# Optimization experiments

Measured on AMD Instinct MI355X. Metric: run time of the kernel, lower is better.

The kernel has to match this reference:

```python
import jax, jax.numpy as jnp
import numpy as np

N, E = 100000, 3200000
IN, HID, OUT = 512, 256, 64
K, ALPHA = 10, 0.1


def setup_inputs() -> dict:
    key = jax.random.key(0)
    k1, k2, k3, k4, k5, k6 = jax.random.split(key, 6)
    x = jax.random.normal(k1, (N, IN), dtype=jnp.float32)
    edge_index = jax.random.randint(k2, (2, E), 0, N, dtype=jnp.int64)
    s1 = 1.0 / np.sqrt(IN)
    s2 = 1.0 / np.sqrt(HID)
    # nn.Linear default init: U(-1/sqrt(fan_in), 1/sqrt(fan_in))
    W1 = jax.random.uniform(k3, (IN, HID), jnp.float32, -s1, s1)
    b1 = jax.random.uniform(k4, (HID,), jnp.float32, -s1, s1)
    W2 = jax.random.uniform(k5, (HID, OUT), jnp.float32, -s2, s2)
    b2 = jax.random.uniform(k6, (OUT,), jnp.float32, -s2, s2)
    return {"x": x, "edge_index": edge_index, "W1": W1, "b1": b1, "W2": W2, "b2": b2}


def reference(x, edge_index, W1, b1, W2, b2):
    # MLP (dropout is identity in eval mode)
    h = jax.nn.relu(x @ W1 + b1) @ W2 + b2  # [N, OUT]

    # gcn_norm with self-loops (PyG APPNP default, normalize=True)
    loop = jnp.arange(N, dtype=edge_index.dtype)
    src = jnp.concatenate([edge_index[0], loop])  # message sources
    dst = jnp.concatenate([edge_index[1], loop])  # aggregation targets
    deg = jax.ops.segment_sum(jnp.ones_like(dst, dtype=h.dtype), dst, num_segments=N)
    dinv = jnp.where(deg > 0, jax.lax.rsqrt(jnp.maximum(deg, 1.0)), 0.0)
    norm = (dinv[src] * dinv[dst])[:, None]  # [E+N, 1]

    x0 = h
    def step(hk, _):
        agg = jax.ops.segment_sum(norm * hk[src], dst, num_segments=N)
        return (1.0 - ALPHA) * agg + ALPHA * x0, None

    h, _ = jax.lax.scan(step, h, None, length=K)
    return h
```

## Files before the change

### kernel.cpp

```cpp
#include <hip/hip_runtime.h>
#include <hip/hip_bf16.h>

#define IN_F  512
#define HID_F 256
#define OUT_F 64

#define BSHIFT 7
#define BNODES 128
#define EBUF_CAP 8192
#define CURS 16

typedef __attribute__((ext_vector_type(8))) short bf16x8;
typedef __attribute__((ext_vector_type(4))) float f32x4;

__device__ inline unsigned short f2bf(float f) {
    unsigned u = __float_as_uint(f);
    u += 0x7FFFu + ((u >> 16) & 1u);
    return (unsigned short)(u >> 16);
}
__device__ inline float bf2f(unsigned short u) {
    return __uint_as_float(((unsigned)u) << 16);
}

__device__ inline bf16x8 cvt8(float4 v0, float4 v1) {
    bf16x8 r;
    r[0] = (short)f2bf(v0.x); r[1] = (short)f2bf(v0.y);
    r[2] = (short)f2bf(v0.z); r[3] = (short)f2bf(v0.w);
    r[4] = (short)f2bf(v1.x); r[5] = (short)f2bf(v1.y);
    r[6] = (short)f2bf(v1.z); r[7] = (short)f2bf(v1.w);
    return r;
}

__device__ inline void gload_lds16(const void* g, void* l) {
    __builtin_amdgcn_global_load_lds(
        (const __attribute__((address_space(1))) void*)g,
        (__attribute__((address_space(3))) void*)l, 16, 0, 0);
}

__global__ void prep_w_kernel(const float* __restrict__ W1,
                              const float* __restrict__ W2,
                              unsigned short* __restrict__ W1T,
                              unsigned short* __restrict__ W2T)
{
    int i = blockIdx.x * 256 + threadIdx.x;
    if (i < IN_F * HID_F) {
        int k = i / HID_F, n = i % HID_F;
        W1T[n * IN_F + k] = f2bf(W1[i]);
    }
    if (i < HID_F * OUT_F) {
        int k = i / OUT_F, n = i % OUT_F;
        W2T[n * HID_F + k] = f2bf(W2[i]);
    }
}

__global__ __launch_bounds__(256) void mlp_kernel(
    const float* __restrict__ x, const unsigned short* __restrict__ W1T,
    const float* __restrict__ b1, const unsigned short* __restrict__ W2T,
    const float* __restrict__ b2, const float* __restrict__ dinv,
    unsigned short* __restrict__ h0bf, unsigned short* __restrict__ g0, int N)
{
    __shared__ uint4 smem4[2048];
    char* smem = (char*)smem4;

    const int t  = threadIdx.x;
    const int w  = t >> 6;
    const int l  = t & 63;
    const int lr = l & 15;
    const int lq = l >> 4;
    const int wr = w & 1;
    const int wc = w >> 1;

    const int row0 = blockIdx.x * 64;

    f32x4 acc[2][8];
    #pragma unroll
    for (int s = 0; s < 2; ++s)
        #pragma unroll
        for (int f = 0; f < 8; ++f) acc[s][f] = (f32x4){0.f, 0.f, 0.f, 0.f};

    const int ar0 = row0 + wr * 32 + lr;
    const int ar1 = ar0 + 16;
    const bool av0 = ar0 < N, av1 = ar1 < N;
    const float* xp0 = x + (size_t)ar0 * IN_F + lq * 8;
    const float* xp1 = x + (size_t)ar1 * IN_F + lq * 8;

    for (int ks = 0; ks < 8; ++ks) {
        if (ks) __syncthreads();
        #pragma unroll
        for (int is = 0; is < 8; ++is) {
            int j  = is * 256 + t;
            int n  = j >> 3;
            int cs = (j & 7) ^ (n & 7);
            const unsigned short* src = W1T + (size_t)n * IN_F + ks * 64 + cs * 8;
            char* dst = smem + is * 4096 + (t >> 6) * 1024;
            gload_lds16(src, dst);
        }
        __syncthreads();

        #pragma unroll
        for (int kh = 0; kh < 2; ++kh) {
            const int kofs = ks * 64 + kh * 32;
            bf16x8 a0, a1;
            if (av0) {
                a0 = cvt8(*(const float4*)(xp0 + kofs),
                          *(const float4*)(xp0 + kofs + 4));
            } else {
                #pragma unroll
                for (int j = 0; j < 8; ++j) a0[j] = 0;
            }
            if (av1) {
                a1 = cvt8(*(const float4*)(xp1 + kofs),
                          *(const float4*)(xp1 + kofs + 4));
            } else {
                #pragma unroll
                for (int j = 0; j < 8; ++j) a1[j] = 0;
            }
            #pragma unroll
            for (int f = 0; f < 8; ++f) {
                int n = wc * 128 + f * 16 + lr;
                unsigned off = (unsigned)(n * 128 + kh * 64 + lq * 16);
                bf16x8 b = *(const bf16x8*)(smem + (off ^ ((unsigned)(n & 7) << 4)));
                acc[0][f] = __builtin_amdgcn_mfma_f32_16x16x32_bf16(a0, b, acc[0][f], 0, 0, 0);
                acc[1][f] = __builtin_amdgcn_mfma_f32_16x16x32_bf16(a1, b, acc[1][f], 0, 0, 0);
            }
        }
    }
    __syncthreads();

    #pragma unroll
    for (int f = 0; f < 8; ++f) {
        int c = wc * 128 + f * 16 + lr;
        float bb = b1[c];
        #pragma unroll
        for (int sub = 0; sub < 2; ++sub) {
            #pragma unroll
            for (int j2 = 0; j2 < 4; ++j2) {
                int r = wr * 32 + sub * 16 + lq * 4 + j2;
                float vv = acc[sub][f][j2] + bb;
                vv = vv > 0.f ? vv : 0.f;
                unsigned off = (unsigned)(r * 512 + c * 2);
                *(unsigned short*)(smem + (off ^ ((unsigned)(r & 7) << 4))) = f2bf(vv);
            }
        }
    }
    __syncthreads();

    f32x4 a2[4];
    #pragma unroll
    for (int m = 0; m < 4; ++m) a2[m] = (f32x4){0.f, 0.f, 0.f, 0.f};

    const unsigned short* w2p = W2T + (size_t)(w * 16 + lr) * HID_F + lq * 8;

    #pragma unroll 2
    for (int ks = 0; ks < 8; ++ks) {
        bf16x8 bfrag = *(const bf16x8*)(w2p + ks * 32);
        #pragma unroll
        for (int m = 0; m < 4; ++m) {
            int r = m * 16 + lr;
            unsigned off = (unsigned)(r * 512 + ks * 64 + lq * 16);
            bf16x8 afrag = *(const bf16x8*)(smem + (off ^ ((unsigned)(r & 7) << 4)));
            a2[m] = __builtin_amdgcn_mfma_f32_16x16x32_bf16(afrag, bfrag, a2[m], 0, 0, 0);
        }
    }

    float bb2 = b2[w * 16 + lr];
    #pragma unroll
    for (int m = 0; m < 4; ++m) {
        #pragma unroll
        for (int j2 = 0; j2 < 4; ++j2) {
            int r = row0 + m * 16 + lq * 4 + j2;
            if (r < N) {
                float v = a2[m][j2] + bb2;
                int c = w * 16 + lr;
                h0bf[(size_t)r * OUT_F + c] = f2bf(v);
                g0[(size_t)r * OUT_F + c]   = f2bf(dinv[r] * v);
            }
        }
    }
}

__global__ __launch_bounds__(256) void bucket_scatter_kernel(
    const int* __restrict__ src, const int* __restrict__ dst,
    int* __restrict__ bcur, unsigned* __restrict__ ebuf, int E)
{
    int stride = gridDim.x * 256;
    for (int e = blockIdx.x * 256 + threadIdx.x; e < E; e += stride) {
        int d = dst[e];
        int b = d >> BSHIFT;
        int pos = atomicAdd(&bcur[b * CURS], 1);
        if (pos < EBUF_CAP)
            ebuf[(size_t)b * EBUF_CAP + pos] =
                ((unsigned)(d & (BNODES - 1)) << 24) | (unsigned)src[e];
    }
}

__global__ __launch_bounds__(1024) void bucket_scan_kernel(
    const int* __restrict__ bcur, int* __restrict__ bbase,
    int* __restrict__ off, int nbk, int N, int E)
{
    __shared__ int sm[1024];
    int t = threadIdx.x;
    int v = 0;
    if (t < nbk) {
        v = bcur[t * CURS];
        if (v > EBUF_CAP) v = EBUF_CAP;
    }
    sm[t] = v;
    __syncthreads();
    for (int ofs = 1; ofs < 1024; ofs <<= 1) {
        int x = (t >= ofs) ? sm[t - ofs] : 0;
        __syncthreads();
        sm[t] += x;
        __syncthreads();
    }
    if (t < nbk) bbase[t] = sm[t] - v;
    if (t == nbk - 1) bbase[nbk] = sm[t];
    if (t == 0) off[N] = E;
}

__global__ __launch_bounds__(256) void bucket_build_kernel(
    const unsigned* __restrict__ ebuf, const int* __restrict__ bbase,
    float* __restrict__ dinv, int* __restrict__ off,
    int* __restrict__ csr, int N)
{
    __shared__ int cnt[BNODES];
    __shared__ int loc[BNODES];
    const int b = blockIdx.x;
    const int t = threadIdx.x;
    const int beg = bbase[b];
    const int nE  = bbase[b + 1] - beg;
    const unsigned* eb = ebuf + (size_t)b * EBUF_CAP;

    if (t < BNODES) cnt[t] = 0;
    __syncthreads();
    for (int j = t; j < nE; j += 256)
        atomicAdd(&cnt[eb[j] >> 24], 1);
    __syncthreads();

    if (t < BNODES) loc[t] = cnt[t];
    __syncthreads();
    for (int ofs = 1; ofs < BNODES; ofs <<= 1) {
        int x = 0;
        if (t < BNODES && t >= ofs) x = loc[t - ofs];
        __syncthreads();
        if (t < BNODES) loc[t] += x;
        __syncthreads();
    }
    if (t < BNODES) {
        int excl = loc[t] - cnt[t];
        int node = b * BNODES + t;
        if (node < N) {
            dinv[node] = rsqrtf((float)(cnt[t] + 1));
            off[node]  = beg + excl;
        }
        loc[t] = beg + excl;
    }
    __syncthreads();
    for (int j = t; j < nE; j += 256) {
        unsigned u = eb[j];
        int pos = atomicAdd(&loc[u >> 24], 1);
        csr[pos] = (int)(u & 0x00FFFFFFu);
    }
}

__global__ __launch_bounds__(256) void step_kernel(
    const unsigned short* __restrict__ gin,
    const unsigned short* __restrict__ h0bf,
    unsigned short* __restrict__ gout, float* __restrict__ outf,
    const int* __restrict__ off, const int* __restrict__ csr,
    const float* __restrict__ dinv, int N, int last)
{
    const int t    = threadIdx.x;
    const int wid  = (blockIdx.x * 256 + t) >> 6;
    if (wid >= N) return;
    const int lane = t & 63;
    const int q    = lane >> 4;
    const int fb   = lane & 15;

    const uint2* gin2 = (const uint2*)gin;

    float a0 = 0.f, a1 = 0.f, a2 = 0.f, a3 = 0.f;
    const int beg = __builtin_amdgcn_readfirstlane(off[wid]);
    const int end = __builtin_amdgcn_readfirstlane(off[wid + 1]);

    for (int i = beg; i < end; i += 32) {
        int idx[8];
        #pragma unroll
        for (int jj = 0; jj < 8; ++jj) {
            int e = i + jj * 4 + q;
            idx[jj] = (e < end) ? csr[e] : -1;
        }
        uint2 v[8];
        #pragma unroll
        for (int jj = 0; jj < 8; ++jj) {
            v[jj] = (idx[jj] >= 0) ? gin2[(size_t)idx[jj] * 16 + fb]
                                   : make_uint2(0u, 0u);
        }
        #pragma unroll
        for (int jj = 0; jj < 8; ++jj) {
            a0 += bf2f((unsigned short)(v[jj].x & 0xffff));
            a1 += bf2f((unsigned short)(v[jj].x >> 16));
            a2 += bf2f((unsigned short)(v[jj].y & 0xffff));
            a3 += bf2f((unsigned short)(v[jj].y >> 16));
        }
    }

    a0 += __shfl_xor(a0, 16); a0 += __shfl_xor(a0, 32);
    a1 += __shfl_xor(a1, 16); a1 += __shfl_xor(a1, 32);
    a2 += __shfl_xor(a2, 16); a2 += __shfl_xor(a2, 32);
    a3 += __shfl_xor(a3, 16); a3 += __shfl_xor(a3, 32);

    if (q == 0) {
        uint2 sv = gin2[(size_t)wid * 16 + fb];
        uint2 hv = ((const uint2*)h0bf)[(size_t)wid * 16 + fb];
        float dv = dinv[wid];
        float s0 = a0 + bf2f((unsigned short)(sv.x & 0xffff));
        float s1 = a1 + bf2f((unsigned short)(sv.x >> 16));
        float s2 = a2 + bf2f((unsigned short)(sv.y & 0xffff));
        float s3 = a3 + bf2f((unsigned short)(sv.y >> 16));
        float r0 = 0.9f * dv * s0 + 0.1f * bf2f((unsigned short)(hv.x & 0xffff));
        float r1 = 0.9f * dv * s1 + 0.1f * bf2f((unsigned short)(hv.x >> 16));
        float r2 = 0.9f * dv * s2 + 0.1f * bf2f((unsigned short)(hv.y & 0xffff));
        float r3 = 0.9f * dv * s3 + 0.1f * bf2f((unsigned short)(hv.y >> 16));
        if (last) {
            float4 o = make_float4(r0, r1, r2, r3);
            *(float4*)(outf + (size_t)wid * OUT_F + fb * 4) = o;
        } else {
            uint2 g;
            g.x = (unsigned)f2bf(dv * r0) | ((unsigned)f2bf(dv * r1) << 16);
            g.y = (unsigned)f2bf(dv * r2) | ((unsigned)f2bf(dv * r3) << 16);
            ((uint2*)gout)[(size_t)wid * 16 + fb] = g;
        }
    }
}

extern "C" void kernel_launch(void* const* d_in, const int* in_sizes, int n_in,
                              void* d_out, int out_size, void* d_ws, size_t ws_size,
                              hipStream_t stream)
{
    const float* x  = (const float*)d_in[0];
    const int*   ei = (const int*)d_in[1];
    const float* W1 = (const float*)d_in[2];
    const float* b1 = (const float*)d_in[3];
    const float* W2 = (const float*)d_in[4];
    const float* b2 = (const float*)d_in[5];
    float* out = (float*)d_out;

    const int N = in_sizes[0] / IN_F;
    const int E = in_sizes[1] / 2;
    const int* src = ei;
    const int* dst = ei + E;
    const int nbk = (N + BNODES - 1) >> BSHIFT;

    char* wsp = (char*)d_ws;
    auto alloc = [&](size_t bytes) -> char* {
        char* p = wsp;
        wsp += (bytes + 255) & ~(size_t)255;
        return p;
    };
    int*   off  = (int*)  alloc((size_t)(N + 1) * 4);
    float* dinv = (float*)alloc((size_t)N * 4);
    int*   csr  = (int*)  alloc((size_t)E * 4);
    unsigned* ebuf = (unsigned*)alloc((size_t)nbk * EBUF_CAP * 4);
    int*   bcur  = (int*) alloc((size_t)nbk * CURS * 4);
    int*   bbase = (int*) alloc((size_t)(nbk + 1) * 4);
    unsigned short* h0bf = (unsigned short*)alloc((size_t)N * OUT_F * 2);
    unsigned short* gA   = (unsigned short*)alloc((size_t)N * OUT_F * 2);
    unsigned short* gB   = (unsigned short*)alloc((size_t)N * OUT_F * 2);
    unsigned short* W1T  = (unsigned short*)alloc((size_t)IN_F * HID_F * 2);
    unsigned short* W2T  = (unsigned short*)alloc((size_t)HID_F * OUT_F * 2);

    hipMemsetAsync(bcur, 0, (size_t)nbk * CURS * 4, stream);

    bucket_scatter_kernel<<<1024, 256, 0, stream>>>(src, dst, bcur, ebuf, E);
    bucket_scan_kernel<<<1, 1024, 0, stream>>>(bcur, bbase, off, nbk, N, E);
    bucket_build_kernel<<<nbk, 256, 0, stream>>>(ebuf, bbase, dinv, off, csr, N);

    prep_w_kernel<<<(IN_F * HID_F + 255) / 256, 256, 0, stream>>>(W1, W2, W1T, W2T);
    mlp_kernel<<<(N + 63) / 64, 256, 0, stream>>>(x, W1T, b1, W2T, b2, dinv,
                                                  h0bf, gA, N);

    const int gS = (N + 3) / 4;
    const unsigned short* gin = gA;
    unsigned short* gout = gB;
    for (int k = 0; k < 10; ++k) {
        int last = (k == 9);
        step_kernel<<<gS, 256, 0, stream>>>(gin, h0bf, gout, out, off, csr,
                                            dinv, N, last);
        const unsigned short* tmp = gin;
        gin = gout;
        gout = (unsigned short*)tmp;
    }
}
```

Measured before the change: 902.1 us.

## Use block-local histogram binning for edge scatter with larger buckets

The edge scatter now processes a chunk of 8192 edges per block. It builds a shared-memory histogram of destination buckets and reserves each bucket's range with one global atomic per bucket per block, instead of one global atomic per edge. Buckets grow from 128 to 512 nodes, so there are fewer of them (up to 256), and the packed edge format uses 17 bits for the source node. The build kernel's scan is adapted to 512 nodes with two entries per thread. This targets global atomic contention in CSR construction, at the cost of more shared-memory work and reading dst twice.

Result: faster. 782.8 us (-13.2%).

```diff
diff --git a/kernel.cpp b/kernel.cpp
--- a/kernel.cpp
+++ b/kernel.cpp
@@ -5,10 +5,12 @@
 #define HID_F 256
 #define OUT_F 64
 
-#define BSHIFT 7
-#define BNODES 128
-#define EBUF_CAP 8192
+#define BSHIFT 9
+#define BNODES 512
+#define NBK_MAX 256
+#define EBUF_CAP 18432
 #define CURS 16
+#define CHUNK 8192
 
 typedef __attribute__((ext_vector_type(8))) short bf16x8;
 typedef __attribute__((ext_vector_type(4))) float f32x4;
@@ -179,18 +181,38 @@
     }
 }
 
-__global__ __launch_bounds__(256) void bucket_scatter_kernel(
+__global__ __launch_bounds__(256) void binned_scatter_kernel(
     const int* __restrict__ src, const int* __restrict__ dst,
-    int* __restrict__ bcur, unsigned* __restrict__ ebuf, int E)
-{
-    int stride = gridDim.x * 256;
-    for (int e = blockIdx.x * 256 + threadIdx.x; e < E; e += stride) {
-        int d = dst[e];
+    int* __restrict__ bcur, unsigned* __restrict__ ebuf, int E, int nbk)
+{
+    __shared__ int hist[NBK_MAX];
+    __shared__ int gbase[NBK_MAX];
+    __shared__ int lcur[NBK_MAX];
+
+    const int t  = threadIdx.x;
+    const int bs = blockIdx.x * CHUNK;
+    const int nE = min(CHUNK, E - bs);
+
+    if (t < NBK_MAX) { hist[t] = 0; lcur[t] = 0; }
+    __syncthreads();
+
+    for (int j = t; j < nE; j += 256)
+        atomicAdd(&hist[dst[bs + j] >> BSHIFT], 1);
+    __syncthreads();
+
+    for (int b = t; b < nbk; b += 256)
+        gbase[b] = hist[b] ? atomicAdd(&bcur[b * CURS], hist[b]) : 0;
+    __syncthreads();
+
+    for (int j = t; j < nE; j += 256) {
+        int d = dst[bs + j];
+        int s = src[bs + j];
         int b = d >> BSHIFT;
-        int pos = atomicAdd(&bcur[b * CURS], 1);
+        int r = atomicAdd(&lcur[b], 1);
+        unsigned pos = (unsigned)(gbase[b] + r);
         if (pos < EBUF_CAP)
             ebuf[(size_t)b * EBUF_CAP + pos] =
-                ((unsigned)(d & (BNODES - 1)) << 24) | (unsigned)src[e];
+                ((unsigned)(d & (BNODES - 1)) << 17) | (unsigned)s;
     }
 }
 
@@ -225,41 +247,45 @@
 {
     __shared__ int cnt[BNODES];
     __shared__ int loc[BNODES];
+    __shared__ int tsum[256];
     const int b = blockIdx.x;
     const int t = threadIdx.x;
     const int beg = bbase[b];
     const int nE  = bbase[b + 1] - beg;
     const unsigned* eb = ebuf + (size_t)b * EBUF_CAP;
 
-    if (t < BNODES) cnt[t] = 0;
+    cnt[t] = 0; cnt[t + 256] = 0;
     __syncthreads();
     for (int j = t; j < nE; j += 256)
-        atomicAdd(&cnt[eb[j] >> 24], 1);
-    __syncthreads();
-
-    if (t < BNODES) loc[t] = cnt[t];
-    __syncthreads();
-    for (int ofs = 1; ofs < BNODES; ofs <<= 1) {
-        int x = 0;
-        if (t < BNODES && t >= ofs) x = loc[t - ofs];
+        atomicAdd(&cnt[eb[j] >> 17], 1);
+    __syncthreads();
+
+    int c0 = cnt[2 * t], c1 = cnt[2 * t + 1];
+    tsum[t] = c0 + c1;
+    __syncthreads();
+    for (int ofs = 1; ofs < 256; ofs <<= 1) {
+        int v = (t >= ofs) ? tsum[t - ofs] : 0;
         __syncthreads();
-        if (t < BNODES) loc[t] += x;
+        tsum[t] += v;
         __syncthreads();
     }
-    if (t < BNODES) {
-        int excl = loc[t] - cnt[t];
-        int node = b * BNODES + t;
+    int base = (t == 0) ? 0 : tsum[t - 1];
+    loc[2 * t]     = beg + base;
+    loc[2 * t + 1] = beg + base + c0;
+    __syncthreads();
+
+    for (int u = t; u < BNODES; u += 256) {
+        int node = b * BNODES + u;
         if (node < N) {
-            dinv[node] = rsqrtf((float)(cnt[t] + 1));
-            off[node]  = beg + excl;
-        }
-        loc[t] = beg + excl;
+            dinv[node] = rsqrtf((float)(cnt[u] + 1));
+            off[node]  = loc[u];
+        }
     }
     __syncthreads();
     for (int j = t; j < nE; j += 256) {
         unsigned u = eb[j];
-        int pos = atomicAdd(&loc[u >> 24], 1);
-        csr[pos] = (int)(u & 0x00FFFFFFu);
+        int pos = atomicAdd(&loc[u >> 17], 1);
+        csr[pos] = (int)(u & 0x1FFFFu);
     }
 }
 
@@ -372,7 +398,8 @@
 
     hipMemsetAsync(bcur, 0, (size_t)nbk * CURS * 4, stream);
 
-    bucket_scatter_kernel<<<1024, 256, 0, stream>>>(src, dst, bcur, ebuf, E);
+    const int gScat = (E + CHUNK - 1) / CHUNK;
+    binned_scatter_kernel<<<gScat, 256, 0, stream>>>(src, dst, bcur, ebuf, E, nbk);
     bucket_scan_kernel<<<1, 1024, 0, stream>>>(bcur, bbase, off, nbk, N, E);
     bucket_build_kernel<<<nbk, 256, 0, stream>>>(ebuf, bbase, dinv, off, csr, N);
 
```
